# Kernel optimization log

Measured on AMD Instinct MI355X. Metric: run time of the kernel, lower is better.

## Reference

```python
import jax, jax.numpy as jnp
import numpy as np

B, N, D = 4, 4096, 512
E = 4 * D            # expanded_dim = 2048
TAIL = E // 2        # tail_dim = 1024
HALF = TAIL // 2     # mt_half = 512
HEAD = E - TAIL      # head_dim = 1024
EPS_RMS = 1e-6
EPS_NORM = 1e-12


def setup_inputs() -> dict:
    key = jax.random.key(0)
    k = jax.random.split(key, 6)
    x = jax.random.normal(k[0], (B, N, D), dtype=jnp.float32)
    g = jnp.ones((D,), dtype=jnp.float32)                                   # RMSNorm gain
    W1 = jax.random.normal(k[1], (D, E), dtype=jnp.float32) * 0.02          # Enricher linear
    b1 = jnp.zeros((E,), dtype=jnp.float32)
    V = jax.random.normal(k[2], (N, N), dtype=jnp.float32) * 0.02           # learned positional matrix slice
    bias = jnp.zeros((HALF,), dtype=jnp.float32)                            # contextualizer bias
    Wf = jax.random.normal(k[3], (HEAD + HALF, D), dtype=jnp.float32) * 0.02  # Fuser linear (no bias)
    return {"x": x, "g": g, "W1": W1, "b1": b1, "V": V, "bias": bias, "Wf": Wf}


def reference(x, g, W1, b1, V, bias, Wf):
    # RMSNorm
    xn = x * jax.lax.rsqrt(jnp.mean(jnp.square(x), axis=-1, keepdims=True) + EPS_RMS) * g
    # Enricher: relu(linear)^2
    enriched = jnp.square(jax.nn.relu(xn @ W1 + b1))                        # [B, N, E]
    head = enriched[..., :HEAD]                                             # [B, N, HEAD]
    tail = enriched[..., HEAD:]                                             # [B, N, TAIL]
    # Contextualizer
    x_left = tail[..., :HALF]
    x_right = tail[..., HALF:]
    nrm = jnp.sqrt(jnp.sum(jnp.square(x_right), axis=-1, keepdims=True))
    xr_n = x_right / jnp.maximum(nrm, EPS_NORM)                             # F.normalize, p=2
    cos = jnp.einsum('bnd,bmd->bnm', xr_n, xr_n)                            # [B, N, N] cosine sim
    weighted = V[None, :, :] * cos                                          # elementwise learned V
    ctx = jnp.einsum('bnm,bmd->bnd', weighted, xr_n)                        # chunked-path bmm uses x_right_norm
    ctx = jax.nn.sigmoid(ctx + bias)
    gated = x_left * ctx                                                    # [B, N, HALF]
    # Fuser + residual
    out = jnp.concatenate([head, gated], axis=-1) @ Wf                      # [B, N, D]
    return x + out
```

## Files before the change

kernel.cpp:

```cpp
#include <hip/hip_runtime.h>
#include <stdint.h>

typedef unsigned short u16;
typedef unsigned long long u64;
typedef __attribute__((ext_vector_type(8))) short bf16x8;
typedef __attribute__((ext_vector_type(4))) float f32x4;
typedef __attribute__((ext_vector_type(16))) float f32x16;
typedef __attribute__((ext_vector_type(4))) unsigned int u32x4;
typedef __attribute__((ext_vector_type(4))) unsigned short u16x4;

#define DEV static __device__ __forceinline__

DEV u16 f2bf(float f){
  unsigned u = __builtin_bit_cast(unsigned, f);
  u += 0x7fffu + ((u >> 16) & 1u);
  return (u16)(u >> 16);
}
DEV float bf2f(u16 v){
  unsigned u = ((unsigned)v) << 16;
  return __builtin_bit_cast(float, u);
}
DEV float bitf(unsigned u){ return __builtin_bit_cast(float, u); }

DEV void async_lds16(const void* g, void* l){
  __builtin_amdgcn_global_load_lds(
      (const __attribute__((address_space(1))) unsigned int*)g,
      (__attribute__((address_space(3))) unsigned int*)l, 16, 0, 0);
}

DEV f32x4 mfma16(bf16x8 a, bf16x8 b, f32x4 c){
  return __builtin_amdgcn_mfma_f32_16x16x32_bf16(a, b, c, 0, 0, 0);
}
DEV f32x16 mfma32(bf16x8 a, bf16x8 b, f32x16 c){
  return __builtin_amdgcn_mfma_f32_32x32x16_bf16(a, b, c, 0, 0, 0);
}

__global__ __launch_bounds__(256) void k_rms(const float* __restrict__ x,
                                             const float* __restrict__ g,
                                             u16* __restrict__ xn){
  const int row = (blockIdx.x << 2) + (threadIdx.x >> 6);
  const int l = threadIdx.x & 63;
  const float* xr = x + (size_t)row * 512 + l * 8;
  f32x4 a = *(const f32x4*)xr;
  f32x4 c = *(const f32x4*)(xr + 4);
  float s = a[0]*a[0]+a[1]*a[1]+a[2]*a[2]+a[3]*a[3]
          + c[0]*c[0]+c[1]*c[1]+c[2]*c[2]+c[3]*c[3];
  #pragma unroll
  for (int off = 32; off >= 1; off >>= 1) s += __shfl_xor(s, off);
  float sc = rsqrtf(s * (1.f/512.f) + 1e-6f);
  f32x4 g0 = *(const f32x4*)&g[l*8];
  f32x4 g1 = *(const f32x4*)&g[l*8+4];
  u32x4 o;
  o[0] = (unsigned)f2bf(a[0]*sc*g0[0]) | ((unsigned)f2bf(a[1]*sc*g0[1]) << 16);
  o[1] = (unsigned)f2bf(a[2]*sc*g0[2]) | ((unsigned)f2bf(a[3]*sc*g0[3]) << 16);
  o[2] = (unsigned)f2bf(c[0]*sc*g1[0]) | ((unsigned)f2bf(c[1]*sc*g1[1]) << 16);
  o[3] = (unsigned)f2bf(c[2]*sc*g1[2]) | ((unsigned)f2bf(c[3]*sc*g1[3]) << 16);
  *(u32x4*)&xn[(size_t)row*512 + l*8] = o;
}

__global__ __launch_bounds__(256) void k_norm(const u16* __restrict__ xr_in,
                                              u16* __restrict__ xrn){
  const int row = (blockIdx.x << 2) + (threadIdx.x >> 6);
  const int l = threadIdx.x & 63;
  u16x4 ha = *(const u16x4*)&xr_in[(size_t)row*512 + l*8];
  u16x4 hb = *(const u16x4*)&xr_in[(size_t)row*512 + l*8 + 4];
  float v[8];
  v[0]=bf2f(ha[0]); v[1]=bf2f(ha[1]); v[2]=bf2f(ha[2]); v[3]=bf2f(ha[3]);
  v[4]=bf2f(hb[0]); v[5]=bf2f(hb[1]); v[6]=bf2f(hb[2]); v[7]=bf2f(hb[3]);
  float s = 0.f;
  #pragma unroll
  for (int i = 0; i < 8; ++i) s += v[i]*v[i];
  #pragma unroll
  for (int off = 32; off >= 1; off >>= 1) s += __shfl_xor(s, off);
  float sc = 1.f / fmaxf(sqrtf(s), 1e-12f);
  u32x4 o;
  o[0] = (unsigned)f2bf(v[0]*sc) | ((unsigned)f2bf(v[1]*sc) << 16);
  o[1] = (unsigned)f2bf(v[2]*sc) | ((unsigned)f2bf(v[3]*sc) << 16);
  o[2] = (unsigned)f2bf(v[4]*sc) | ((unsigned)f2bf(v[5]*sc) << 16);
  o[3] = (unsigned)f2bf(v[6]*sc) | ((unsigned)f2bf(v[7]*sc) << 16);
  *(u32x4*)&xrn[(size_t)row*512 + l*8] = o;
}

__global__ __launch_bounds__(256) void k_tr32(const float* __restrict__ in,
                                              u16* __restrict__ out, int R, int C){
  __shared__ float tile[32][33];
  const int t = threadIdx.x;
  const int r = t >> 3;
  const int c4 = (t & 7) << 2;
  const int r0 = blockIdx.y << 5, c0 = blockIdx.x << 5;
  f32x4 v = *(const f32x4*)&in[(size_t)(r0 + r) * C + c0 + c4];
  tile[r][c4+0]=v[0]; tile[r][c4+1]=v[1]; tile[r][c4+2]=v[2]; tile[r][c4+3]=v[3];
  __syncthreads();
  u64 o =
      (u64)f2bf(tile[c4+0][r])
    | ((u64)f2bf(tile[c4+1][r]) << 16)
    | ((u64)f2bf(tile[c4+2][r]) << 32)
    | ((u64)f2bf(tile[c4+3][r]) << 48);
  *(u64*)&out[(size_t)(c0 + r) * R + r0 + c4] = o;
}

__global__ __launch_bounds__(256) void k_trb(const u16* __restrict__ in,
                                             u16* __restrict__ out, int R, int C){
  __shared__ u16 tile[32][40];
  const int t = threadIdx.x;
  const int r = t >> 3;
  const int c4 = (t & 7) << 2;
  const size_t bb = (size_t)blockIdx.z * R * C;
  const int r0 = blockIdx.y << 5, c0 = blockIdx.x << 5;
  u64 v = *(const u64*)&in[bb + (size_t)(r0 + r)*C + c0 + c4];
  tile[r][c4+0]=(u16)v; tile[r][c4+1]=(u16)(v>>16);
  tile[r][c4+2]=(u16)(v>>32); tile[r][c4+3]=(u16)(v>>48);
  __syncthreads();
  u64 o =
      (u64)tile[c4+0][r]
    | ((u64)tile[c4+1][r] << 16)
    | ((u64)tile[c4+2][r] << 32)
    | ((u64)tile[c4+3][r] << 48);
  *(u64*)&out[bb + (size_t)(c0 + r) * R + r0 + c4] = o;
}

__global__ __launch_bounds__(256) void k_gemm1(const u16* __restrict__ A,
                                               const u16* __restrict__ Bt,
                                               const float* __restrict__ b1,
                                               u16* __restrict__ head,
                                               u16* __restrict__ xleft,
                                               u16* __restrict__ xright){
  __shared__ u16 As[2][128*32];
  __shared__ u16 Bs[2][128*32];
  const int t = threadIdx.x;
  const int l = t & 63;
  const int w = t >> 6;
  const int wr = w >> 1, wc = w & 1;
  const int m0 = blockIdx.x << 7;
  const int n0 = blockIdx.y << 7;
  const int ra = t >> 2;
  const int kb = (t & 3) << 3;
  const int lr = l & 15, lh = l >> 4;
  f32x4 acc[4][4];
  #pragma unroll
  for (int i=0;i<4;i++)
    #pragma unroll
    for (int j=0;j<4;j++)
      #pragma unroll
      for (int r=0;r<4;r++) acc[i][j][r] = 0.f;

  async_lds16(A  + (size_t)(m0 + ra)*512      + kb, &As[0][t*8]);
  async_lds16(A  + (size_t)(m0 + 64 + ra)*512 + kb, &As[0][2048 + t*8]);
  async_lds16(Bt + (size_t)(n0 + ra)*512      + kb, &Bs[0][t*8]);
  async_lds16(Bt + (size_t)(n0 + 64 + ra)*512 + kb, &Bs[0][2048 + t*8]);
  __syncthreads();

  int cur = 0;
  for (int k0 = 0; k0 < 512; k0 += 32){
    if (k0 + 32 < 512){
      const int kn = k0 + 32;
      const int nb = cur ^ 1;
      async_lds16(A  + (size_t)(m0 + ra)*512      + kn + kb, &As[nb][t*8]);
      async_lds16(A  + (size_t)(m0 + 64 + ra)*512 + kn + kb, &As[nb][2048 + t*8]);
      async_lds16(Bt + (size_t)(n0 + ra)*512      + kn + kb, &Bs[nb][t*8]);
      async_lds16(Bt + (size_t)(n0 + 64 + ra)*512 + kn + kb, &Bs[nb][2048 + t*8]);
    }
    bf16x8 af[4], bfr[4];
    #pragma unroll
    for (int i=0;i<4;i++){
      af[i]  = *(const bf16x8*)&As[cur][(wr*64 + i*16 + lr)*32 + lh*8];
      bfr[i] = *(const bf16x8*)&Bs[cur][(wc*64 + i*16 + lr)*32 + lh*8];
    }
    #pragma unroll
    for (int i=0;i<4;i++)
      #pragma unroll
      for (int j=0;j<4;j++)
        acc[i][j] = mfma16(af[i], bfr[j], acc[i][j]);
    __syncthreads();
    cur ^= 1;
  }
  #pragma unroll
  for (int i=0;i<4;i++){
    #pragma unroll
    for (int j=0;j<4;j++){
      int c = n0 + wc*64 + j*16 + lr;
      float bb = b1[c];
      #pragma unroll
      for (int r=0;r<4;r++){
        int m = m0 + wr*64 + i*16 + lh*4 + r;
        float v = acc[i][j][r] + bb;
        v = v > 0.f ? v*v : 0.f;
        if (c < 1024)      head[(size_t)m*1024 + c] = f2bf(v);
        else if (c < 1536) xleft[(size_t)m*512 + (c - 1024)] = f2bf(v);
        else               xright[(size_t)m*512 + (c - 1536)] = f2bf(v);
      }
    }
  }
}

__global__ __launch_bounds__(256) void k_gemm3(const u16* __restrict__ head,
                                               const u16* __restrict__ gated,
                                               const u16* __restrict__ Wft,
                                               const float* __restrict__ x,
                                               float* __restrict__ out){
  __shared__ u16 As[2][128*32];
  __shared__ u16 Bs[2][128*32];
  const int t = threadIdx.x;
  const int l = t & 63;
  const int w = t >> 6;
  const int wr = w >> 1, wc = w & 1;
  const int m0 = blockIdx.x << 7;
  const int n0 = blockIdx.y << 7;
  const int ra = t >> 2;
  const int kb = (t & 3) << 3;
  const int lr = l & 15, lh = l >> 4;
  f32x4 acc[4][4];
  #pragma unroll
  for (int i=0;i<4;i++)
    #pragma unroll
    for (int j=0;j<4;j++)
      #pragma unroll
      for (int r=0;r<4;r++) acc[i][j][r] = 0.f;

  auto stage = [&](int nb, int k0){
    const u16* sa; size_t lda; int kk;
    if (k0 < 1024){ sa = head;  lda = 1024; kk = k0; }
    else          { sa = gated; lda = 512;  kk = k0 - 1024; }
    async_lds16(sa + (size_t)(m0 + ra)*lda      + kk + kb, &As[nb][t*8]);
    async_lds16(sa + (size_t)(m0 + 64 + ra)*lda + kk + kb, &As[nb][2048 + t*8]);
    async_lds16(Wft + (size_t)(n0 + ra)*1536      + k0 + kb, &Bs[nb][t*8]);
    async_lds16(Wft + (size_t)(n0 + 64 + ra)*1536 + k0 + kb, &Bs[nb][2048 + t*8]);
  };
  stage(0, 0);
  __syncthreads();

  int cur = 0;
  for (int k0 = 0; k0 < 1536; k0 += 32){
    if (k0 + 32 < 1536) stage(cur ^ 1, k0 + 32);
    bf16x8 af[4], bfr[4];
    #pragma unroll
    for (int i=0;i<4;i++){
      af[i]  = *(const bf16x8*)&As[cur][(wr*64 + i*16 + lr)*32 + lh*8];
      bfr[i] = *(const bf16x8*)&Bs[cur][(wc*64 + i*16 + lr)*32 + lh*8];
    }
    #pragma unroll
    for (int i=0;i<4;i++)
      #pragma unroll
      for (int j=0;j<4;j++)
        acc[i][j] = mfma16(af[i], bfr[j], acc[i][j]);
    __syncthreads();
    cur ^= 1;
  }
  #pragma unroll
  for (int i=0;i<4;i++){
    #pragma unroll
    for (int j=0;j<4;j++){
      int c = n0 + wc*64 + j*16 + lr;
      #pragma unroll
      for (int r=0;r<4;r++){
        int m = m0 + wr*64 + i*16 + lh*4 + r;
        size_t gi = (size_t)m*512 + c;
        out[gi] = x[gi] + acc[i][j][r];
      }
    }
  }
}

__global__ __launch_bounds__(512, 2) void k_attn(const u16* __restrict__ xrn,
                                                 const u16* __restrict__ xrT,
                                                 const float* __restrict__ V,
                                                 const float* __restrict__ bias,
                                                 const u16* __restrict__ xleft,
                                                 u16* __restrict__ gated){
  __shared__ char smem[154624];
  char* km = smem;
  char* tt = smem + 65536;
  char* ps = smem + 131072;
  char* pb = smem + 149504;
  const int t = threadIdx.x;
  const int l = t & 63, w = t >> 6;
  const int wr = w >> 2, ks = w & 3, wc = (w >> 1) & 1, kq2 = w & 1;
  const int lo = l & 31, hi = l >> 5;
  const int bid = blockIdx.x;
  const int b  = (bid & 7) >> 1;
  const int n0 = ((((bid >> 3) << 1) | (bid & 1))) << 6;
  const u16* xb  = xrn + (size_t)b * (4096*512);
  const u16* xTb = xrT + (size_t)b * (512*4096);

  bf16x8 areg[8];
  {
    const u16* apt = xb + (size_t)(n0 + wr*32 + lo)*512 + ks*128 + hi*8;
    #pragma unroll
    for (int kq = 0; kq < 8; ++kq) areg[kq] = *(const bf16x8*)(apt + kq*16);
  }
  f32x16 acc[8];
  #pragma unroll
  for (int i = 0; i < 8; ++i)
    #pragma unroll
    for (int j = 0; j < 16; ++j) acc[i][j] = 0.f;

  const int prf = t >> 3;
  const int pc4 = (t & 7) << 2;
  const int wrr = prf >> 5, prr = prf & 31;

  #pragma unroll
  for (int c = 0; c < 4; ++c){
    int off = (c*512 + t)*16;
    int row = off >> 10, colb = off & 1023;
    async_lds16(xb + (size_t)row*512 + ((colb ^ ((row&7)<<4)) >> 1), km + off);
    int dr = off >> 6, cb2 = off & 63;
    async_lds16(xTb + (size_t)dr*4096 + ((cb2 ^ ((dr&6)<<3)) >> 1), tt + off);
  }
  __syncthreads();

  int cur = 0;
  for (int it = 0; it < 128; ++it){
    const int m0 = it << 5;
    f32x4 vf = *(const f32x4*)&V[(size_t)(n0 + prf)*4096 + m0 + pc4];
    if (it < 127){
      const int m1 = m0 + 32;
      const int nb = (cur ^ 1) * 32768;
      #pragma unroll
      for (int c = 0; c < 4; ++c){
        int off = (c*512 + t)*16;
        int row = off >> 10, colb = off & 1023;
        async_lds16(xb + (size_t)(m1 + row)*512 + ((colb ^ ((row&7)<<4)) >> 1),
                    km + nb + off);
        int dr = off >> 6, cb2 = off & 63;
        async_lds16(xTb + (size_t)dr*4096 + m1 + ((cb2 ^ ((dr&6)<<3)) >> 1),
                    tt + nb + off);
      }
    }
    f32x16 S0, S1;
    #pragma unroll
    for (int j = 0; j < 16; ++j){ S0[j] = 0.f; S1[j] = 0.f; }
    {
      const char* kbp = km + cur*32768 + lo*1024;
      const int swk = (lo & 7) << 4;
      #pragma unroll
      for (int kq = 0; kq < 8; kq += 2){
        bf16x8 b0 = *(const bf16x8*)(kbp + ((ks*256 + kq*32 + hi*16) ^ swk));
        bf16x8 b1 = *(const bf16x8*)(kbp + ((ks*256 + (kq+1)*32 + hi*16) ^ swk));
        S0 = mfma32(areg[kq],   b0, S0);
        S1 = mfma32(areg[kq+1], b1, S1);
      }
    }
    {
      char* pw = ps + ((wr*4 + ks)*32)*72 + lo*2;
      #pragma unroll
      for (int rg = 0; rg < 16; ++rg){
        int prow = (rg & 3) + 8*(rg >> 2) + 4*hi;
        *(u16*)(pw + prow*72) = f2bf(S0[rg] + S1[rg]);
      }
    }
    asm volatile("s_waitcnt lgkmcnt(0)" ::: "memory");
    __builtin_amdgcn_s_barrier();
    __builtin_amdgcn_sched_barrier(0);
    {
      float s0=0.f, s1=0.f, s2=0.f, s3=0.f;
      #pragma unroll
      for (int k2 = 0; k2 < 4; ++k2){
        u16x4 pv = *(const u16x4*)(ps + (((wrr*4 + k2)*32 + prr)*36 + pc4)*2);
        s0 += bf2f(pv[0]); s1 += bf2f(pv[1]); s2 += bf2f(pv[2]); s3 += bf2f(pv[3]);
      }
      u64 po = (u64)f2bf(s0 * vf[0])
             | ((u64)f2bf(s1 * vf[1]) << 16)
             | ((u64)f2bf(s2 * vf[2]) << 32)
             | ((u64)f2bf(s3 * vf[3]) << 48);
      *(u64*)(pb + (prf*40 + pc4)*2) = po;
    }
    asm volatile("s_waitcnt lgkmcnt(0)" ::: "memory");
    __builtin_amdgcn_s_barrier();
    __builtin_amdgcn_sched_barrier(0);
    {
      bf16x8 pa = *(const bf16x8*)(pb + (wr*32 + lo)*80 + kq2*32 + hi*16);
      const char* tb = tt + cur*32768;
      #pragma unroll
      for (int ds = 0; ds < 8; ++ds){
        int drow = wc*256 + ds*32 + lo;
        bf16x8 bfr = *(const bf16x8*)(tb + drow*64 +
                       ((kq2*32 + hi*16) ^ ((drow & 6) << 3)));
        acc[ds] = mfma32(pa, bfr, acc[ds]);
      }
    }
    __syncthreads();
    cur ^= 1;
  }

  float* red = (float*)smem;
  const int rbase = (wr*2 + wc) * 8192;
  if (kq2 == 1){
    #pragma unroll
    for (int ds = 0; ds < 8; ++ds)
      #pragma unroll
      for (int rg = 0; rg < 16; ++rg)
        red[rbase + (ds*16 + rg)*64 + l] = acc[ds][rg];
  }
  __syncthreads();
  if (kq2 == 0){
    #pragma unroll
    for (int ds = 0; ds < 8; ++ds){
      const int d = wc*256 + ds*32 + lo;
      const float bs = bias[d];
      #pragma unroll
      for (int rg = 0; rg < 16; ++rg){
        int row = n0 + wr*32 + (rg & 3) + 8*(rg >> 2) + 4*hi;
        float v = acc[ds][rg] + red[rbase + (ds*16 + rg)*64 + l] + bs;
        v = 1.f / (1.f + __expf(-v));
        size_t gi = (size_t)(b*4096 + row)*512 + d;
        gated[gi] = f2bf(bf2f(xleft[gi]) * v);
      }
    }
  }
}

extern "C" void kernel_launch(void* const* d_in, const int* in_sizes, int n_in,
                              void* d_out, int out_size, void* d_ws, size_t ws_size,
                              hipStream_t stream){
  const float* x    = (const float*)d_in[0];
  const float* g    = (const float*)d_in[1];
  const float* W1   = (const float*)d_in[2];
  const float* b1   = (const float*)d_in[3];
  const float* V    = (const float*)d_in[4];
  const float* bias = (const float*)d_in[5];
  const float* Wf   = (const float*)d_in[6];
  float* out = (float*)d_out;

  char* ws = (char*)d_ws;
  const size_t MB = 1024u*1024u;
  u16*   xn     = (u16*)  (ws + 0*MB);
  u16*   W1t    = (u16*)  (ws + 16*MB);
  u16*   Wft    = (u16*)  (ws + 18*MB);
  u16*   head   = (u16*)  (ws + 20*MB);
  u16*   xleft  = (u16*)  (ws + 52*MB);
  u16*   xright = (u16*)  (ws + 68*MB);
  u16*   gated  = (u16*)  (ws + 68*MB);
  u16*   xrn    = (u16*)  (ws + 84*MB);
  u16*   xrT    = (u16*)  (ws + 100*MB);

  k_rms  <<<dim3(4096),       dim3(256), 0, stream>>>(x, g, xn);
  k_tr32 <<<dim3(64, 16),     dim3(256), 0, stream>>>(W1, W1t, 512, 2048);
  k_tr32 <<<dim3(16, 48),     dim3(256), 0, stream>>>(Wf, Wft, 1536, 512);
  k_gemm1<<<dim3(128, 16),    dim3(256), 0, stream>>>(xn, W1t, b1, head, xleft, xright);
  k_norm <<<dim3(4096),       dim3(256), 0, stream>>>(xright, xrn);
  k_trb  <<<dim3(16, 128, 4), dim3(256), 0, stream>>>(xrn, xrT, 4096, 512);
  k_attn <<<dim3(256),        dim3(512), 0, stream>>>(xrn, xrT, V, bias, xleft, gated);
  k_gemm3<<<dim3(128, 4),     dim3(256), 0, stream>>>(head, gated, Wft, x, out);
}
```

Before: 370.0 us.

## Fuse partial-S reduction into MFMA A-operand load and drop barrier stage

The V matrix is pre-transposed into bf16 by a new transpose kernel, so each lane can load the V values matching its own MFMA A-fragment positions. Each lane then sums the four k-split partial S tiles straight from LDS into its A-operand registers. This removes the intermediate pb buffer, one LDS round trip and one block barrier per iteration. The costs are an extra 4096x4096 transpose launch each call, strided 2-byte global loads of V, and launch bounds relaxed to one block per CU.

```diff
diff --git a/kernel.cpp b/kernel.cpp
--- a/kernel.cpp
+++ b/kernel.cpp
@@ -261,17 +261,16 @@
   }
 }
 
-__global__ __launch_bounds__(512, 2) void k_attn(const u16* __restrict__ xrn,
+__global__ __launch_bounds__(512, 1) void k_attn(const u16* __restrict__ xrn,
                                                  const u16* __restrict__ xrT,
-                                                 const float* __restrict__ V,
+                                                 const u16* __restrict__ Vt,
                                                  const float* __restrict__ bias,
                                                  const u16* __restrict__ xleft,
                                                  u16* __restrict__ gated){
-  __shared__ char smem[154624];
+  __shared__ char smem[149504];
   char* km = smem;
   char* tt = smem + 65536;
   char* ps = smem + 131072;
-  char* pb = smem + 149504;
   const int t = threadIdx.x;
   const int l = t & 63, w = t >> 6;
   const int wr = w >> 2, ks = w & 3, wc = (w >> 1) & 1, kq2 = w & 1;
@@ -294,9 +293,7 @@
     #pragma unroll
     for (int j = 0; j < 16; ++j) acc[i][j] = 0.f;
 
-  const int prf = t >> 3;
-  const int pc4 = (t & 7) << 2;
-  const int wrr = prf >> 5, prr = prf & 31;
+  const u16* vtb = Vt + (size_t)(kq2*16 + hi*8)*4096 + n0 + wr*32 + lo;
 
   #pragma unroll
   for (int c = 0; c < 4; ++c){
@@ -311,7 +308,9 @@
   int cur = 0;
   for (int it = 0; it < 128; ++it){
     const int m0 = it << 5;
-    f32x4 vf = *(const f32x4*)&V[(size_t)(n0 + prf)*4096 + m0 + pc4];
+    u16 vt[8];
+    #pragma unroll
+    for (int e = 0; e < 8; ++e) vt[e] = vtb[(size_t)(m0 + e)*4096];
     if (it < 127){
       const int m1 = m0 + 32;
       const int nb = (cur ^ 1) * 32768;
@@ -351,24 +350,26 @@
     asm volatile("s_waitcnt lgkmcnt(0)" ::: "memory");
     __builtin_amdgcn_s_barrier();
     __builtin_amdgcn_sched_barrier(0);
+    bf16x8 pa;
     {
-      float s0=0.f, s1=0.f, s2=0.f, s3=0.f;
-      #pragma unroll
-      for (int k2 = 0; k2 < 4; ++k2){
-        u16x4 pv = *(const u16x4*)(ps + (((wrr*4 + k2)*32 + prr)*36 + pc4)*2);
-        s0 += bf2f(pv[0]); s1 += bf2f(pv[1]); s2 += bf2f(pv[2]); s3 += bf2f(pv[3]);
-      }
-      u64 po = (u64)f2bf(s0 * vf[0])
-             | ((u64)f2bf(s1 * vf[1]) << 16)
-             | ((u64)f2bf(s2 * vf[2]) << 32)
-             | ((u64)f2bf(s3 * vf[3]) << 48);
-      *(u64*)(pb + (prf*40 + pc4)*2) = po;
-    }
-    asm volatile("s_waitcnt lgkmcnt(0)" ::: "memory");
-    __builtin_amdgcn_s_barrier();
-    __builtin_amdgcn_sched_barrier(0);
+      const char* pr = ps + ((wr*4)*32 + lo)*72 + kq2*32 + hi*16;
+      u32x4 q0 = *(const u32x4*)(pr + 0*2304);
+      u32x4 q1 = *(const u32x4*)(pr + 1*2304);
+      u32x4 q2 = *(const u32x4*)(pr + 2*2304);
+      u32x4 q3 = *(const u32x4*)(pr + 3*2304);
+      u32x4 pk;
+      #pragma unroll
+      for (int j = 0; j < 4; ++j){
+        float se = bitf(q0[j] << 16) + bitf(q1[j] << 16)
+                 + bitf(q2[j] << 16) + bitf(q3[j] << 16);
+        float so = bitf(q0[j] & 0xffff0000u) + bitf(q1[j] & 0xffff0000u)
+                 + bitf(q2[j] & 0xffff0000u) + bitf(q3[j] & 0xffff0000u);
+        pk[j] = (unsigned)f2bf(se * bf2f(vt[2*j]))
+              | ((unsigned)f2bf(so * bf2f(vt[2*j+1])) << 16);
+      }
+      pa = __builtin_bit_cast(bf16x8, pk);
+    }
     {
-      bf16x8 pa = *(const bf16x8*)(pb + (wr*32 + lo)*80 + kq2*32 + hi*16);
       const char* tb = tt + cur*32768;
       #pragma unroll
       for (int ds = 0; ds < 8; ++ds){
@@ -432,13 +433,15 @@
   u16*   gated  = (u16*)  (ws + 68*MB);
   u16*   xrn    = (u16*)  (ws + 84*MB);
   u16*   xrT    = (u16*)  (ws + 100*MB);
+  u16*   Vtb    = (u16*)  (ws + 116*MB);
 
   k_rms  <<<dim3(4096),       dim3(256), 0, stream>>>(x, g, xn);
+  k_tr32 <<<dim3(128, 128),   dim3(256), 0, stream>>>(V, Vtb, 4096, 4096);
   k_tr32 <<<dim3(64, 16),     dim3(256), 0, stream>>>(W1, W1t, 512, 2048);
   k_tr32 <<<dim3(16, 48),     dim3(256), 0, stream>>>(Wf, Wft, 1536, 512);
   k_gemm1<<<dim3(128, 16),    dim3(256), 0, stream>>>(xn, W1t, b1, head, xleft, xright);
   k_norm <<<dim3(4096),       dim3(256), 0, stream>>>(xright, xrn);
   k_trb  <<<dim3(16, 128, 4), dim3(256), 0, stream>>>(xrn, xrT, 4096, 512);
-  k_attn <<<dim3(256),        dim3(512), 0, stream>>>(xrn, xrT, V, bias, xleft, gated);
+  k_attn <<<dim3(256),        dim3(512), 0, stream>>>(xrn, xrT, Vtb, bias, xleft, gated);
   k_gemm3<<<dim3(128, 4),     dim3(256), 0, stream>>>(head, gated, Wft, x, out);
 }
```

Measured after the change: 505.0 us. 1.36x slower.
